# Performance work log

Measured on AMD Instinct MI355X. Metric: run time of the kernel, lower is better.

The kernel has to match this reference:

```python
import jax, jax.numpy as jnp
import numpy as np

B, D, SLOTS, TOPK, CODE, ANCH = 8192, 64, 32, 3, 128, 32
BETA = 0.25  # vq_commitment_beta


def _clinear(zr, zi, Wr, Wi, br, bi):
    # ComplexLinear: real = Wr(zr)-Wi(zi), imag = Wi(zr)+Wr(zi); each nn.Linear carries its own bias
    return (zr @ Wr + br) - (zi @ Wi + bi), (zr @ Wi + bi) + (zi @ Wr + br)


def _layernorm(x, g, b, eps=1e-6):
    m = x.mean(-1, keepdims=True)
    v = ((x - m) ** 2).mean(-1, keepdims=True)  # biased var, as torch LayerNorm
    return (x - m) / jnp.sqrt(v + eps) * g + b


def setup_inputs() -> dict:
    key = jax.random.key(0)
    ks = jax.random.split(key, 16)
    f = jax.random.normal
    s = 0.05
    rng_init = 1.0 / np.sqrt(D)
    return dict(
        curr_r=f(ks[0], (B, D)), curr_i=f(ks[1], (B, D)),
        mem_r=f(ks[2], (B, SLOTS, D)), mem_i=f(ks[3], (B, SLOTS, D)),
        codebook=jax.random.uniform(ks[4], (CODE, 2 * D), minval=-rng_init, maxval=rng_init),
        qkv_Wr=f(ks[5], (3, D, D)) * s, qkv_Wi=f(ks[6], (3, D, D)) * s,
        qkv_br=jnp.zeros((3, D)), qkv_bi=jnp.zeros((3, D)),
        quad_Wr=f(ks[7], (D, D)) * s, quad_Wi=f(ks[8], (D, D)) * s,
        quad_br=jnp.zeros((D,)), quad_bi=jnp.zeros((D,)),
        sens_Wr=f(ks[9], (D, D)) * s, sens_Wi=f(ks[10], (D, D)) * s,
        sens_br=jnp.zeros((D,)), sens_bi=jnp.zeros((D,)),
        vis_palette=f(ks[11], (ANCH, 2 * D)), aud_palette=f(ks[12], (ANCH, 2 * D)),
        gate_W=f(ks[13], (2 * D, 1)) * s, gate_b=jnp.zeros((1,)),
        addr_W=f(ks[14], (2 * D, SLOTS)) * s, addr_b=jnp.zeros((SLOTS,)),
        ln_gamma_r=jnp.ones((D,)), ln_beta_r=jnp.zeros((D,)),
        ln_gamma_i=jnp.ones((D,)), ln_beta_i=jnp.zeros((D,)),
    )


def reference(curr_r, curr_i, mem_r, mem_i, codebook,
              qkv_Wr, qkv_Wi, qkv_br, qkv_bi,
              quad_Wr, quad_Wi, quad_br, quad_bi,
              sens_Wr, sens_Wi, sens_br, sens_bi,
              vis_palette, aud_palette,
              gate_W, gate_b, addr_W, addr_b,
              ln_gamma_r, ln_beta_r, ln_gamma_i, ln_beta_i):
    sg = jax.lax.stop_gradient
    z_flat = jnp.concatenate([curr_r, curr_i], -1)  # [B,2D]

    # ---- EMA_VQ (eval path): argmin codebook lookup + straight-through ----
    d = (z_flat ** 2).sum(1, keepdims=True) + (codebook ** 2).sum(1) - 2.0 * z_flat @ codebook.T
    d = jnp.maximum(d, 0.0)
    indices = jnp.argmin(d, -1)                      # [B]
    z_q = codebook[indices]                          # [B,2D]
    vq_loss = BETA * ((sg(z_q) - z_flat) ** 2).mean(-1)
    z_q = z_flat + sg(z_q - z_flat)
    probs = jnp.zeros((CODE,), z_flat.dtype).at[indices].add(1.0) / B
    norm_entropy = -(probs * jnp.log(probs + 1e-10)).sum() / np.log(CODE)
    vq_r, vq_i = z_q[..., :D], z_q[..., D:]

    # ---- HermitianGating ----
    qr, qi = _clinear(curr_r, curr_i, qkv_Wr[0], qkv_Wi[0], qkv_br[0], qkv_bi[0])
    kr, ki = _clinear(curr_r, curr_i, qkv_Wr[1], qkv_Wi[1], qkv_br[1], qkv_bi[1])
    vr, vi = _clinear(curr_r, curr_i, qkv_Wr[2], qkv_Wi[2], qkv_br[2], qkv_bi[2])
    gate = jax.nn.sigmoid((qr * kr + qi * ki).sum(-1, keepdims=True))
    g_r, g_i = vr * gate, vi * gate

    # ---- AssociativeMemory: softmax read + topk scatter write ----
    sim = jnp.einsum('bsd,bd->bs', mem_r, curr_r) + jnp.einsum('bsd,bd->bs', mem_i, curr_i)
    sim = sim - sg(sim.max(-1, keepdims=True))
    attn = jax.nn.softmax(sim, -1)
    read_r = jnp.einsum('bs,bsd->bd', attn, mem_r)
    read_i = jnp.einsum('bs,bsd->bd', attn, mem_i)
    write_gate = jax.nn.sigmoid(z_flat @ gate_W + gate_b)[:, :, None]  # [B,1,1]
    logits = z_flat @ addr_W + addr_b
    logits = logits - sg(logits.max(-1, keepdims=True))
    ww = jax.nn.softmax(logits, -1)                  # [B,SLOTS]
    slot_entropy = (-(ww * jnp.log(ww + 1e-10)).sum(-1)).mean()
    top_vals, top_idx = jax.lax.top_k(ww, TOPK)
    sparse = jnp.zeros_like(ww).at[jnp.arange(B)[:, None], top_idx].set(top_vals)
    sparse = sparse / (sparse.sum(-1, keepdims=True) + 1e-6)
    eff = write_gate * sparse[..., None]             # [B,SLOTS,1]
    nm_r = jnp.tanh(mem_r + eff * (curr_r[:, None, :] - mem_r))
    nm_i = jnp.tanh(mem_i + eff * (curr_i[:, None, :] - mem_i))
    nm_r = _layernorm(nm_r, ln_gamma_r, ln_beta_r)
    nm_i = _layernorm(nm_i, ln_gamma_i, ln_beta_i)

    # ---- SubmodalityAnchorModule ----
    s_r, s_i = _clinear(curr_r, curr_i, sens_Wr, sens_Wi, sens_br, sens_bi)
    sflat = jnp.concatenate([s_r, s_i], -1)

    def attend(pal):
        sc = sflat @ pal.T
        sc = sc - sg(sc.max(-1, keepdims=True))
        return jax.nn.softmax(sc, -1) @ pal

    vis = attend(vis_palette)
    aud = attend(aud_palette)
    exp_r = vis[..., :D] - aud[..., D:]   # vis_c + i*aud_c
    exp_i = vis[..., D:] + aud[..., :D]

    # ---- QuadratureModule: multiply by i ----
    zr, zi = _clinear(curr_r, curr_i, quad_Wr, quad_Wi, quad_br, quad_bi)
    q_r, q_i = -zi, zr

    combined = jnp.concatenate(
        [vq_r, vq_i, g_r, g_i, read_r, read_i, exp_r, exp_i, q_r, q_i,
         nm_r.reshape(B, -1), nm_i.reshape(B, -1)], -1)  # [B, 10*D + 2*SLOTS*D]
    return combined, vq_loss, indices, slot_entropy, norm_entropy
```

## Files before the change

### kernel.cpp

```cpp
#include <hip/hip_runtime.h>
#include <hip/hip_bf16.h>


#define NROWS 8
#define NBLOCKS 1024
#define RSTRIDE 4736

static constexpr size_t OFF_VQLOSS = 38797312UL;
static constexpr size_t OFF_IDX    = 38805504UL;
static constexpr size_t OFF_SENT   = 38813696UL;
static constexpr size_t OFF_NENT   = 38813697UL;

struct Params {
  const float* curr_r; const float* curr_i;
  const float* mem_r;  const float* mem_i;
  const float* codebook;
  const float* qkv_Wr; const float* qkv_Wi; const float* qkv_br; const float* qkv_bi;
  const float* quad_Wr; const float* quad_Wi; const float* quad_br; const float* quad_bi;
  const float* sens_Wr; const float* sens_Wi; const float* sens_br; const float* sens_bi;
  const float* vis_pal; const float* aud_pal;
  const float* gate_W; const float* gate_b;
  const float* addr_W; const float* addr_b;
  const float* ln_gr; const float* ln_br; const float* ln_gi; const float* ln_bi;
  float* out;
  int* hist;
  float* rowent;
};

__global__ __launch_bounds__(256) void row_main(Params P) {
  const int b = blockIdx.x;
  const int t = threadIdx.x;
  const int lane = t & 63;
  const int wv = t >> 6;

  __shared__ float zr[64], zi[64];
  __shared__ float s_qr[64], s_qi[64], s_kr[64], s_ki[64], s_vr[64], s_vi[64];
  __shared__ float sfl[128];
  __shared__ float s_sp[4][4][64];
  __shared__ float lp[4][32];
  __shared__ float s_eff[32];
  __shared__ float s_sim[32], s_attn[32];
  __shared__ float s_rr[4][8][8], s_ri[4][8][8];
  __shared__ float s_pv[4][32], s_pa[4][32];
  __shared__ float s_pvp[32], s_pap[32];
  __shared__ float s_vo[128], s_ao[128];
  __shared__ float s_wg, s_gate;

  const size_t bb = (size_t)b;
  const int s = t >> 3, k = t & 7, d0 = k * 8;
  const float* mrp = P.mem_r + ((bb * 32 + s) * 64 + d0);
  const float* mip = P.mem_i + ((bb * 32 + s) * 64 + d0);
  float4 a0 = *(const float4*)mrp, a1 = *(const float4*)(mrp + 4);
  float4 b0 = *(const float4*)mip, b1 = *(const float4*)(mip + 4);
  float mr[8] = {a0.x, a0.y, a0.z, a0.w, a1.x, a1.y, a1.z, a1.w};
  float mi[8] = {b0.x, b0.y, b0.z, b0.w, b1.x, b1.y, b1.z, b1.w};

  if (t < 64)       zr[t]      = P.curr_r[bb * 64 + t];
  else if (t < 128) zi[t - 64] = P.curr_i[bb * 64 + (t - 64)];
  __syncthreads();

  float* orow = P.out + bb * RSTRIDE;

  {
    const int j = lane, cl = wv;
    const float *Wr, *Wi, *br_, *bi_;
    if      (cl == 0) { Wr = P.qkv_Wr;        Wi = P.qkv_Wi;        br_ = P.qkv_br;       bi_ = P.qkv_bi;       }
    else if (cl == 1) { Wr = P.qkv_Wr + 4096; Wi = P.qkv_Wi + 4096; br_ = P.qkv_br + 64;  bi_ = P.qkv_bi + 64;  }
    else if (cl == 2) { Wr = P.qkv_Wr + 8192; Wi = P.qkv_Wi + 8192; br_ = P.qkv_br + 128; bi_ = P.qkv_bi + 128; }
    else              { Wr = P.quad_Wr;       Wi = P.quad_Wi;       br_ = P.quad_br;      bi_ = P.quad_bi;      }
    float aRR = 0.f, aRI = 0.f, aIR = 0.f, aII = 0.f;
    for (int d = 0; d < 64; ++d) {
      const float xr = zr[d], xi = zi[d];
      const float wr = Wr[d * 64 + j], wi = Wi[d * 64 + j];
      aRR += xr * wr; aRI += xr * wi; aIR += xi * wr; aII += xi * wi;
    }
    const float oR = (aRR + br_[j]) - (aII + bi_[j]);
    const float oI = (aRI + bi_[j]) + (aIR + br_[j]);
    if      (cl == 0) { s_qr[j] = oR; s_qi[j] = oI; }
    else if (cl == 1) { s_kr[j] = oR; s_ki[j] = oI; }
    else if (cl == 2) { s_vr[j] = oR; s_vi[j] = oI; }
    else              { orow[512 + j] = -oI; orow[576 + j] = oR; }
    float bRR = 0.f, bRI = 0.f, bIR = 0.f, bII = 0.f;
    for (int dd = 0; dd < 16; ++dd) {
      const int d = wv * 16 + dd;
      const float xr = zr[d], xi = zi[d];
      const float wr = P.sens_Wr[d * 64 + j], wi = P.sens_Wi[d * 64 + j];
      bRR += xr * wr; bRI += xr * wi; bIR += xi * wr; bII += xi * wi;
    }
    s_sp[wv][0][j] = bRR; s_sp[wv][1][j] = bRI; s_sp[wv][2][j] = bIR; s_sp[wv][3][j] = bII;
  }
  __syncthreads();

  {
    float sp = 0.f;
    #pragma unroll
    for (int x = 0; x < 8; ++x) sp += mr[x] * zr[d0 + x] + mi[x] * zi[d0 + x];
    sp += __shfl_xor(sp, 1); sp += __shfl_xor(sp, 2); sp += __shfl_xor(sp, 4);
    if (k == 0) s_sim[s] = sp;
  }
  if (t < 128) {
    const int q = t >> 5, l = t & 31;
    const float* zz = (q < 2) ? zr : zi;
    const int zb = (q & 1) * 32;
    float a = 0.f;
    for (int i = 0; i < 32; ++i) a += zz[zb + i] * P.addr_W[(q * 32 + i) * 32 + l];
    lp[q][l] = a;
  } else if (t < 192) {
    const int j = t - 128;
    float tw = zr[j] * P.gate_W[j] + zi[j] * P.gate_W[64 + j];
    #pragma unroll
    for (int m = 1; m <= 32; m <<= 1) tw += __shfl_xor(tw, m);
    if (j == 0) s_wg = tw;
  } else {
    const int j = t - 192;
    float g = s_qr[j] * s_kr[j] + s_qi[j] * s_ki[j];
    #pragma unroll
    for (int m = 1; m <= 32; m <<= 1) g += __shfl_xor(g, m);
    if (j == 0) s_gate = 1.f / (1.f + expf(-g));
  }
  __syncthreads();

  if (t < 32) {
    float v = s_sim[t];
    float mx = v;
    #pragma unroll
    for (int m = 16; m >= 1; m >>= 1) mx = fmaxf(mx, __shfl_xor(mx, m));
    float e = expf(v - mx);
    float sm = e;
    #pragma unroll
    for (int m = 16; m >= 1; m >>= 1) sm += __shfl_xor(sm, m);
    s_attn[t] = e / sm;
  } else if (t >= 64 && t < 96) {
    const int l = t - 64;
    float lg = lp[0][l] + lp[1][l] + lp[2][l] + lp[3][l] + P.addr_b[l];
    float mx = lg;
    #pragma unroll
    for (int m = 16; m >= 1; m >>= 1) mx = fmaxf(mx, __shfl_xor(mx, m));
    float e = expf(lg - mx);
    float sm = e;
    #pragma unroll
    for (int m = 16; m >= 1; m >>= 1) sm += __shfl_xor(sm, m);
    const float w = e / sm;
    float es = -(w * logf(w + 1e-10f));
    #pragma unroll
    for (int m = 16; m >= 1; m >>= 1) es += __shfl_xor(es, m);
    if (l == 0) P.rowent[b] = es;
    const float myw = w;
    bool picked = false;
    float val = w; int idx = l;
    float sumtop = 0.f;
    #pragma unroll
    for (int it = 0; it < 3; ++it) {
      float v2 = val; int i2 = idx;
      #pragma unroll
      for (int m = 16; m >= 1; m >>= 1) {
        float ov = __shfl_xor(v2, m); int oi = __shfl_xor(i2, m);
        if (ov > v2 || (ov == v2 && oi < i2)) { v2 = ov; i2 = oi; }
      }
      sumtop += v2;
      if (l == i2) { picked = true; val = -1e30f; }
    }
    const float wgate = 1.f / (1.f + expf(-(s_wg + P.gate_b[0])));
    s_eff[l] = picked ? wgate * (myw / (sumtop + 1e-6f)) : 0.f;
  } else if (t >= 128 && t < 192) {
    const int j = t - 128;
    const float aRR = s_sp[0][0][j] + s_sp[1][0][j] + s_sp[2][0][j] + s_sp[3][0][j];
    const float aRI = s_sp[0][1][j] + s_sp[1][1][j] + s_sp[2][1][j] + s_sp[3][1][j];
    const float aIR = s_sp[0][2][j] + s_sp[1][2][j] + s_sp[2][2][j] + s_sp[3][2][j];
    const float aII = s_sp[0][3][j] + s_sp[1][3][j] + s_sp[2][3][j] + s_sp[3][3][j];
    const float oR = (aRR + P.sens_br[j]) - (aII + P.sens_bi[j]);
    const float oI = (aRI + P.sens_bi[j]) + (aIR + P.sens_br[j]);
    sfl[j] = oR; sfl[64 + j] = oI;
  }
  __syncthreads();

  const float aw = s_attn[s];
  {
    float pr[8], pi[8];
    #pragma unroll
    for (int x = 0; x < 8; ++x) { pr[x] = aw * mr[x]; pi[x] = aw * mi[x]; }
    #pragma unroll
    for (int m = 8; m <= 32; m <<= 1) {
      #pragma unroll
      for (int x = 0; x < 8; ++x) { pr[x] += __shfl_xor(pr[x], m); pi[x] += __shfl_xor(pi[x], m); }
    }
    if (lane < 8) {
      #pragma unroll
      for (int x = 0; x < 8; ++x) { s_rr[wv][lane][x] = pr[x]; s_ri[wv][lane][x] = pi[x]; }
    }
  }
  {
    const float eff = s_eff[s];
    float nr[8], ni[8];
    #pragma unroll
    for (int x = 0; x < 8; ++x) {
      nr[x] = tanhf(mr[x] + eff * (zr[d0 + x] - mr[x]));
      ni[x] = tanhf(mi[x] + eff * (zi[d0 + x] - mi[x]));
    }
    float sR = 0.f, sI = 0.f;
    #pragma unroll
    for (int x = 0; x < 8; ++x) { sR += nr[x]; sI += ni[x]; }
    sR += __shfl_xor(sR, 1); sR += __shfl_xor(sR, 2); sR += __shfl_xor(sR, 4);
    sI += __shfl_xor(sI, 1); sI += __shfl_xor(sI, 2); sI += __shfl_xor(sI, 4);
    const float mR = sR * (1.f / 64.f), mI = sI * (1.f / 64.f);
    float vR = 0.f, vI = 0.f;
    #pragma unroll
    for (int x = 0; x < 8; ++x) {
      float dr = nr[x] - mR; vR += dr * dr;
      float di = ni[x] - mI; vI += di * di;
    }
    vR += __shfl_xor(vR, 1); vR += __shfl_xor(vR, 2); vR += __shfl_xor(vR, 4);
    vI += __shfl_xor(vI, 1); vI += __shfl_xor(vI, 2); vI += __shfl_xor(vI, 4);
    const float invR = 1.f / sqrtf(vR * (1.f / 64.f) + 1e-6f);
    const float invI = 1.f / sqrtf(vI * (1.f / 64.f) + 1e-6f);
    float oR[8], oI[8];
    #pragma unroll
    for (int x = 0; x < 8; ++x) {
      const int d = d0 + x;
      oR[x] = (nr[x] - mR) * invR * P.ln_gr[d] + P.ln_br[d];
      oI[x] = (ni[x] - mI) * invI * P.ln_gi[d] + P.ln_bi[d];
    }
    *(float4*)&orow[640 + s * 64 + d0]      = make_float4(oR[0], oR[1], oR[2], oR[3]);
    *(float4*)&orow[640 + s * 64 + d0 + 4]  = make_float4(oR[4], oR[5], oR[6], oR[7]);
    *(float4*)&orow[2688 + s * 64 + d0]     = make_float4(oI[0], oI[1], oI[2], oI[3]);
    *(float4*)&orow[2688 + s * 64 + d0 + 4] = make_float4(oI[4], oI[5], oI[6], oI[7]);
  }
  if (t < 128) {
    const int a = t & 31, q = t >> 5;
    float sc = 0.f;
    for (int x = q * 32; x < q * 32 + 32; ++x) sc += sfl[x] * P.vis_pal[a * 128 + x];
    s_pv[q][a] = sc;
  } else {
    const int tt = t - 128, a = tt & 31, q = tt >> 5;
    float sc = 0.f;
    for (int x = q * 32; x < q * 32 + 32; ++x) sc += sfl[x] * P.aud_pal[a * 128 + x];
    s_pa[q][a] = sc;
  }
  __syncthreads();

  if (t < 64) {
    const int kk = t >> 3, xx = t & 7;
    float rv = s_rr[0][kk][xx] + s_rr[1][kk][xx] + s_rr[2][kk][xx] + s_rr[3][kk][xx];
    float iv = s_ri[0][kk][xx] + s_ri[1][kk][xx] + s_ri[2][kk][xx] + s_ri[3][kk][xx];
    orow[256 + t] = rv;
    orow[320 + t] = iv;
  } else if (t >= 128 && t < 160) {
    const int a = t - 128;
    float sc = s_pv[0][a] + s_pv[1][a] + s_pv[2][a] + s_pv[3][a];
    float mx = sc;
    #pragma unroll
    for (int m = 16; m >= 1; m >>= 1) mx = fmaxf(mx, __shfl_xor(mx, m));
    float e = expf(sc - mx);
    float sm = e;
    #pragma unroll
    for (int m = 16; m >= 1; m >>= 1) sm += __shfl_xor(sm, m);
    s_pvp[a] = e / sm;
  } else if (t >= 192 && t < 224) {
    const int a = t - 192;
    float sc = s_pa[0][a] + s_pa[1][a] + s_pa[2][a] + s_pa[3][a];
    float mx = sc;
    #pragma unroll
    for (int m = 16; m >= 1; m >>= 1) mx = fmaxf(mx, __shfl_xor(mx, m));
    float e = expf(sc - mx);
    float sm = e;
    #pragma unroll
    for (int m = 16; m >= 1; m >>= 1) sm += __shfl_xor(sm, m);
    s_pap[a] = e / sm;
  }
  __syncthreads();

  if (t < 128) {
    float v = 0.f;
    for (int a = 0; a < 32; ++a) v += s_pvp[a] * P.vis_pal[a * 128 + t];
    s_vo[t] = v;
  } else {
    const int j = t - 128;
    float v = 0.f;
    for (int a = 0; a < 32; ++a) v += s_pap[a] * P.aud_pal[a * 128 + j];
    s_ao[j] = v;
  }
  if (t < 64)       orow[128 + t] = s_vr[t] * s_gate;
  else if (t < 128) orow[192 + (t - 64)] = s_vi[t - 64] * s_gate;
  __syncthreads();

  if (t < 64)       orow[384 + t] = s_vo[t] - s_ao[64 + t];
  else if (t < 128) orow[448 + (t - 64)] = s_vo[t] + s_ao[t - 64];
}

__global__ __launch_bounds__(256) void vq_kernel(Params P) {
  const int t = threadIdx.x;
  const int bid = blockIdx.x;
  const int lane = t & 63;
  const int wv = t >> 6;

  __shared__ __align__(16) float s_zr[NROWS][64], s_zi[NROWS][64];
  __shared__ double s_cbn[128];
  __shared__ double s_dall[NROWS][256];
  __shared__ float s_vqls[NROWS];
  __shared__ int s_idx[NROWS];

  {
    const float* cr = P.curr_r + (size_t)bid * (NROWS * 64);
    const float* ci = P.curr_i + (size_t)bid * (NROWS * 64);
    float* zr = &s_zr[0][0];
    float* zi = &s_zi[0][0];
    for (int i = t; i < NROWS * 64; i += 256) { zr[i] = cr[i]; zi[i] = ci[i]; }
  }
  {
    const float* cb = P.codebook + (t & 127) * 128 + (t >> 7) * 64;
    double a = 0.0;
    for (int d = 0; d < 64; ++d) { double w = (double)cb[d]; a = fma(w, w, a); }
    s_dall[0][t] = a;
    __syncthreads();
    if (t < 128) s_cbn[t] = s_dall[0][t] + s_dall[0][t + 128];
    __syncthreads();
  }
  {
    const int c = t & 127, h = t >> 7;
    const float* cb = P.codebook + c * 128 + h * 64;
    const float (*zb)[64] = h ? s_zi : s_zr;
    double acc[NROWS];
    #pragma unroll
    for (int r = 0; r < NROWS; ++r) acc[r] = 0.0;
    for (int d = 0; d < 64; ++d) {
      const double w = (double)cb[d];
      #pragma unroll
      for (int r = 0; r < NROWS; ++r) acc[r] = fma(w, (double)zb[r][d], acc[r]);
    }
    #pragma unroll
    for (int r = 0; r < NROWS; ++r) s_dall[r][h * 128 + c] = acc[r];
    __syncthreads();
    #pragma unroll
    for (int rr = 0; rr < 2; ++rr) {
      const int r = wv * 2 + rr;
      const double d0 = s_cbn[lane]      - 2.0 * (s_dall[r][lane]      + s_dall[r][128 + lane]);
      const double d1 = s_cbn[lane + 64] - 2.0 * (s_dall[r][64 + lane] + s_dall[r][192 + lane]);
      double sv = d0; int si = lane;
      if (d1 < sv) { sv = d1; si = lane + 64; }
      #pragma unroll
      for (int m = 1; m <= 32; m <<= 1) {
        double ov = __shfl_xor(sv, m);
        int oi = __shfl_xor(si, m);
        if (ov < sv || (ov == sv && oi < si)) { sv = ov; si = oi; }
      }
      if (lane == 0) { s_idx[r] = si; atomicAdd(&P.hist[si], 1); }
    }
    __syncthreads();
  }
  {
    #pragma unroll
    for (int rr = 0; rr < 2; ++rr) {
      const int r = wv * 2 + rr;
      const float* cb = P.codebook + (size_t)s_idx[r] * 128;
      float d0_ = cb[lane] - s_zr[r][lane];
      float d1_ = cb[64 + lane] - s_zi[r][lane];
      float v = d0_ * d0_ + d1_ * d1_;
      #pragma unroll
      for (int m = 1; m <= 32; m <<= 1) v += __shfl_xor(v, m);
      if (lane == 0) s_vqls[r] = 0.25f * v * (1.0f / 128.0f);
    }
  }
  __syncthreads();
  {
    const int j = t & 63, g = t >> 6;
    #pragma unroll
    for (int rr = 0; rr < 4; ++rr) {
      const int r = (g >> 1) * 4 + rr;
      float* orow = P.out + ((size_t)bid * NROWS + r) * RSTRIDE;
      const float* cb = P.codebook + (size_t)s_idx[r] * 128;
      if ((g & 1) == 0) {
        float z = s_zr[r][j];
        orow[j] = z + (cb[j] - z);
      } else {
        float z = s_zi[r][j];
        orow[64 + j] = z + (cb[64 + j] - z);
      }
    }
  }
  if (t < NROWS) {
    P.out[OFF_VQLOSS + (size_t)bid * NROWS + t] = s_vqls[t];
    P.out[OFF_IDX + (size_t)bid * NROWS + t] = (float)s_idx[t];
  }
}

__global__ __launch_bounds__(256) void finalize_k(const int* hist, const float* rowent,
                                                  float* out) {
  const int t = threadIdx.x;
  __shared__ float red[256];
  float se = 0.f;
  for (int i = t; i < 8192; i += 256) se += rowent[i];
  red[t] = se;
  __syncthreads();
  for (int off = 128; off >= 1; off >>= 1) {
    if (t < off) red[t] += red[t + off];
    __syncthreads();
  }
  if (t == 0) out[OFF_SENT] = red[0] / 8192.0f;
  __syncthreads();
  float ne = 0.f;
  if (t < 128) {
    const float pp = (float)hist[t] / 8192.0f;
    ne = -(pp * logf(pp + 1e-10f));
  }
  red[t] = ne;
  __syncthreads();
  for (int off = 128; off >= 1; off >>= 1) {
    if (t < off) red[t] += red[t + off];
    __syncthreads();
  }
  if (t == 0) out[OFF_NENT] = red[0] / logf(128.0f);
}

extern "C" void kernel_launch(void* const* d_in, const int* in_sizes, int n_in,
                              void* d_out, int out_size, void* d_ws, size_t ws_size,
                              hipStream_t stream) {
  (void)in_sizes; (void)n_in; (void)out_size; (void)ws_size;
  Params P;
  P.curr_r   = (const float*)d_in[0];
  P.curr_i   = (const float*)d_in[1];
  P.mem_r    = (const float*)d_in[2];
  P.mem_i    = (const float*)d_in[3];
  P.codebook = (const float*)d_in[4];
  P.qkv_Wr   = (const float*)d_in[5];
  P.qkv_Wi   = (const float*)d_in[6];
  P.qkv_br   = (const float*)d_in[7];
  P.qkv_bi   = (const float*)d_in[8];
  P.quad_Wr  = (const float*)d_in[9];
  P.quad_Wi  = (const float*)d_in[10];
  P.quad_br  = (const float*)d_in[11];
  P.quad_bi  = (const float*)d_in[12];
  P.sens_Wr  = (const float*)d_in[13];
  P.sens_Wi  = (const float*)d_in[14];
  P.sens_br  = (const float*)d_in[15];
  P.sens_bi  = (const float*)d_in[16];
  P.vis_pal  = (const float*)d_in[17];
  P.aud_pal  = (const float*)d_in[18];
  P.gate_W   = (const float*)d_in[19];
  P.gate_b   = (const float*)d_in[20];
  P.addr_W   = (const float*)d_in[21];
  P.addr_b   = (const float*)d_in[22];
  P.ln_gr    = (const float*)d_in[23];
  P.ln_br    = (const float*)d_in[24];
  P.ln_gi    = (const float*)d_in[25];
  P.ln_bi    = (const float*)d_in[26];
  P.out = (float*)d_out;
  P.hist = (int*)d_ws;
  P.rowent = (float*)((char*)d_ws + 512);

  hipMemsetAsync(d_ws, 0, 512, stream);
  row_main<<<dim3(8192), dim3(256), 0, stream>>>(P);
  vq_kernel<<<dim3(NBLOCKS), dim3(256), 0, stream>>>(P);
  finalize_k<<<dim3(1), dim3(256), 0, stream>>>(P.hist, P.rowent, (float*)d_out);
}
```

Measured before the change: 252.3 us.

## Fuse VQ kernel into per-row kernel processing two rows per block

Result: slower. 277.2 us (+9.9%).

```diff
diff --git a/kernel.cpp b/kernel.cpp
--- a/kernel.cpp
+++ b/kernel.cpp
@@ -2,8 +2,6 @@
 #include <hip/hip_bf16.h>
 
 
-#define NROWS 8
-#define NBLOCKS 1024
 #define RSTRIDE 4736
 
 static constexpr size_t OFF_VQLOSS = 38797312UL;
@@ -27,40 +25,109 @@
   float* rowent;
 };
 
-__global__ __launch_bounds__(256) void row_main(Params P) {
+__global__ __launch_bounds__(256) void row2_kernel(Params P) {
   const int b = blockIdx.x;
   const int t = threadIdx.x;
   const int lane = t & 63;
   const int wv = t >> 6;
 
-  __shared__ float zr[64], zi[64];
-  __shared__ float s_qr[64], s_qi[64], s_kr[64], s_ki[64], s_vr[64], s_vi[64];
-  __shared__ float sfl[128];
-  __shared__ float s_sp[4][4][64];
-  __shared__ float lp[4][32];
-  __shared__ float s_eff[32];
-  __shared__ float s_sim[32], s_attn[32];
-  __shared__ float s_rr[4][8][8], s_ri[4][8][8];
-  __shared__ float s_pv[4][32], s_pa[4][32];
-  __shared__ float s_pvp[32], s_pap[32];
-  __shared__ float s_vo[128], s_ao[128];
-  __shared__ float s_wg, s_gate;
-
-  const size_t bb = (size_t)b;
+  __shared__ float zr[2][64], zi[2][64];
+  __shared__ double s_pd[2][2][128];
+  __shared__ float s_qr[2][64], s_qi[2][64], s_kr[2][64], s_ki[2][64], s_vr[2][64], s_vi[2][64];
+  __shared__ float sfl[2][128];
+  __shared__ float s_sp[4][2][4][64];
+  __shared__ float alg[2][32];
+  __shared__ float s_eff[2][32];
+  __shared__ float s_sim[2][32], s_attn[2][32];
+  __shared__ float s_rr[2][4][8][8], s_ri[2][4][8][8];
+  __shared__ float s_pv[2][4][32], s_pa[2][4][32];
+  __shared__ float s_pvp[2][32], s_pap[2][32];
+  __shared__ float s_vo[2][128], s_ao[2][128];
+  __shared__ float s_wg[2], s_gate[2], s_vqls[2];
+  __shared__ int s_idx[2];
+
+  const size_t r0 = (size_t)b * 2;
+  float* orow0 = P.out + r0 * RSTRIDE;
+  float* orow1 = P.out + (r0 + 1) * RSTRIDE;
+
   const int s = t >> 3, k = t & 7, d0 = k * 8;
-  const float* mrp = P.mem_r + ((bb * 32 + s) * 64 + d0);
-  const float* mip = P.mem_i + ((bb * 32 + s) * 64 + d0);
-  float4 a0 = *(const float4*)mrp, a1 = *(const float4*)(mrp + 4);
-  float4 b0 = *(const float4*)mip, b1 = *(const float4*)(mip + 4);
-  float mr[8] = {a0.x, a0.y, a0.z, a0.w, a1.x, a1.y, a1.z, a1.w};
-  float mi[8] = {b0.x, b0.y, b0.z, b0.w, b1.x, b1.y, b1.z, b1.w};
-
-  if (t < 64)       zr[t]      = P.curr_r[bb * 64 + t];
-  else if (t < 128) zi[t - 64] = P.curr_i[bb * 64 + (t - 64)];
-  __syncthreads();
-
-  float* orow = P.out + bb * RSTRIDE;
-
+  const float* mrp0 = P.mem_r + ((r0)     * 32 + s) * 64 + d0;
+  const float* mip0 = P.mem_i + ((r0)     * 32 + s) * 64 + d0;
+  const float* mrp1 = P.mem_r + ((r0 + 1) * 32 + s) * 64 + d0;
+  const float* mip1 = P.mem_i + ((r0 + 1) * 32 + s) * 64 + d0;
+  float4 a00 = *(const float4*)mrp0, a01 = *(const float4*)(mrp0 + 4);
+  float4 b00 = *(const float4*)mip0, b01 = *(const float4*)(mip0 + 4);
+  float4 a10 = *(const float4*)mrp1, a11 = *(const float4*)(mrp1 + 4);
+  float4 b10 = *(const float4*)mip1, b11 = *(const float4*)(mip1 + 4);
+  float mr0[8] = {a00.x, a00.y, a00.z, a00.w, a01.x, a01.y, a01.z, a01.w};
+  float mi0[8] = {b00.x, b00.y, b00.z, b00.w, b01.x, b01.y, b01.z, b01.w};
+  float mr1[8] = {a10.x, a10.y, a10.z, a10.w, a11.x, a11.y, a11.z, a11.w};
+  float mi1[8] = {b10.x, b10.y, b10.z, b10.w, b11.x, b11.y, b11.z, b11.w};
+
+  if (t < 128) zr[t >> 6][t & 63] = P.curr_r[r0 * 64 + t];
+  else         zi[(t - 128) >> 6][t & 63] = P.curr_i[r0 * 64 + (t - 128)];
+  __syncthreads();
+
+  {
+    const int c = t & 127, h = t >> 7;
+    const float* cb = P.codebook + (size_t)c * 128 + h * 64;
+    const float* z0 = h ? zi[0] : zr[0];
+    const float* z1 = h ? zi[1] : zr[1];
+    double a0 = 0.0, a1 = 0.0;
+    for (int x = 0; x < 64; ++x) {
+      const double w = (double)cb[x];
+      const double e0 = w - (double)z0[x]; a0 = fma(e0, e0, a0);
+      const double e1 = w - (double)z1[x]; a1 = fma(e1, e1, a1);
+    }
+    s_pd[h][0][c] = a0;
+    s_pd[h][1][c] = a1;
+  }
+  __syncthreads();
+
+  if (wv < 2) {
+    const int r = wv;
+    double sv = s_pd[0][r][lane] + s_pd[1][r][lane]; int si = lane;
+    const double dv = s_pd[0][r][lane + 64] + s_pd[1][r][lane + 64];
+    if (dv < sv) { sv = dv; si = lane + 64; }
+    #pragma unroll
+    for (int m = 1; m <= 32; m <<= 1) {
+      double ov = __shfl_xor(sv, m);
+      int oi = __shfl_xor(si, m);
+      if (ov < sv || (ov == sv && oi < si)) { sv = ov; si = oi; }
+    }
+    if (lane == 0) { s_idx[r] = si; atomicAdd(&P.hist[si], 1); }
+  } else if (wv == 2) {
+    const int r = lane >> 5, l = lane & 31;
+    float wg = 0.f;
+    #pragma unroll
+    for (int q4 = 0; q4 < 4; ++q4) {
+      const int jj = l + q4 * 32;
+      const float z = (jj < 64) ? zr[r][jj] : zi[r][jj - 64];
+      wg += z * P.gate_W[jj];
+    }
+    #pragma unroll
+    for (int m = 16; m >= 1; m >>= 1) wg += __shfl_xor(wg, m);
+    if (l == 0) s_wg[r] = wg;
+  } else {
+    const int r = lane >> 5, l = lane & 31;
+    float a = P.addr_b[l];
+    for (int d = 0; d < 64; ++d) a += zr[r][d] * P.addr_W[d * 32 + l];
+    for (int d = 0; d < 64; ++d) a += zi[r][d] * P.addr_W[(64 + d) * 32 + l];
+    alg[r][l] = a;
+  }
+  __syncthreads();
+
+  {
+    float sp0 = 0.f, sp1 = 0.f;
+    #pragma unroll
+    for (int x = 0; x < 8; ++x) {
+      sp0 += mr0[x] * zr[0][d0 + x] + mi0[x] * zi[0][d0 + x];
+      sp1 += mr1[x] * zr[1][d0 + x] + mi1[x] * zi[1][d0 + x];
+    }
+    sp0 += __shfl_xor(sp0, 1); sp0 += __shfl_xor(sp0, 2); sp0 += __shfl_xor(sp0, 4);
+    sp1 += __shfl_xor(sp1, 1); sp1 += __shfl_xor(sp1, 2); sp1 += __shfl_xor(sp1, 4);
+    if (k == 0) { s_sim[0][s] = sp0; s_sim[1][s] = sp1; }
+  }
   {
     const int j = lane, cl = wv;
     const float *Wr, *Wi, *br_, *bi_;
@@ -68,71 +135,66 @@
     else if (cl == 1) { Wr = P.qkv_Wr + 4096; Wi = P.qkv_Wi + 4096; br_ = P.qkv_br + 64;  bi_ = P.qkv_bi + 64;  }
     else if (cl == 2) { Wr = P.qkv_Wr + 8192; Wi = P.qkv_Wi + 8192; br_ = P.qkv_br + 128; bi_ = P.qkv_bi + 128; }
     else              { Wr = P.quad_Wr;       Wi = P.quad_Wi;       br_ = P.quad_br;      bi_ = P.quad_bi;      }
-    float aRR = 0.f, aRI = 0.f, aIR = 0.f, aII = 0.f;
+    float aRR0 = 0.f, aRI0 = 0.f, aIR0 = 0.f, aII0 = 0.f;
+    float aRR1 = 0.f, aRI1 = 0.f, aIR1 = 0.f, aII1 = 0.f;
     for (int d = 0; d < 64; ++d) {
-      const float xr = zr[d], xi = zi[d];
       const float wr = Wr[d * 64 + j], wi = Wi[d * 64 + j];
-      aRR += xr * wr; aRI += xr * wi; aIR += xi * wr; aII += xi * wi;
-    }
-    const float oR = (aRR + br_[j]) - (aII + bi_[j]);
-    const float oI = (aRI + bi_[j]) + (aIR + br_[j]);
-    if      (cl == 0) { s_qr[j] = oR; s_qi[j] = oI; }
-    else if (cl == 1) { s_kr[j] = oR; s_ki[j] = oI; }
-    else if (cl == 2) { s_vr[j] = oR; s_vi[j] = oI; }
-    else              { orow[512 + j] = -oI; orow[576 + j] = oR; }
-    float bRR = 0.f, bRI = 0.f, bIR = 0.f, bII = 0.f;
+      const float xr0 = zr[0][d], xi0 = zi[0][d];
+      const float xr1 = zr[1][d], xi1 = zi[1][d];
+      aRR0 += xr0 * wr; aRI0 += xr0 * wi; aIR0 += xi0 * wr; aII0 += xi0 * wi;
+      aRR1 += xr1 * wr; aRI1 += xr1 * wi; aIR1 += xi1 * wr; aII1 += xi1 * wi;
+    }
+    const float brj = br_[j], bij = bi_[j];
+    const float oR0 = (aRR0 + brj) - (aII0 + bij);
+    const float oI0 = (aRI0 + bij) + (aIR0 + brj);
+    const float oR1 = (aRR1 + brj) - (aII1 + bij);
+    const float oI1 = (aRI1 + bij) + (aIR1 + brj);
+    if      (cl == 0) { s_qr[0][j] = oR0; s_qi[0][j] = oI0; s_qr[1][j] = oR1; s_qi[1][j] = oI1; }
+    else if (cl == 1) { s_kr[0][j] = oR0; s_ki[0][j] = oI0; s_kr[1][j] = oR1; s_ki[1][j] = oI1; }
+    else if (cl == 2) { s_vr[0][j] = oR0; s_vi[0][j] = oI0; s_vr[1][j] = oR1; s_vi[1][j] = oI1; }
+    else { orow0[512 + j] = -oI0; orow0[576 + j] = oR0;
+           orow1[512 + j] = -oI1; orow1[576 + j] = oR1; }
+    float bRR0 = 0.f, bRI0 = 0.f, bIR0 = 0.f, bII0 = 0.f;
+    float bRR1 = 0.f, bRI1 = 0.f, bIR1 = 0.f, bII1 = 0.f;
     for (int dd = 0; dd < 16; ++dd) {
       const int d = wv * 16 + dd;
-      const float xr = zr[d], xi = zi[d];
       const float wr = P.sens_Wr[d * 64 + j], wi = P.sens_Wi[d * 64 + j];
-      bRR += xr * wr; bRI += xr * wi; bIR += xi * wr; bII += xi * wi;
-    }
-    s_sp[wv][0][j] = bRR; s_sp[wv][1][j] = bRI; s_sp[wv][2][j] = bIR; s_sp[wv][3][j] = bII;
-  }
-  __syncthreads();
-
-  {
-    float sp = 0.f;
-    #pragma unroll
-    for (int x = 0; x < 8; ++x) sp += mr[x] * zr[d0 + x] + mi[x] * zi[d0 + x];
-    sp += __shfl_xor(sp, 1); sp += __shfl_xor(sp, 2); sp += __shfl_xor(sp, 4);
-    if (k == 0) s_sim[s] = sp;
-  }
-  if (t < 128) {
-    const int q = t >> 5, l = t & 31;
-    const float* zz = (q < 2) ? zr : zi;
-    const int zb = (q & 1) * 32;
-    float a = 0.f;
-    for (int i = 0; i < 32; ++i) a += zz[zb + i] * P.addr_W[(q * 32 + i) * 32 + l];
-    lp[q][l] = a;
-  } else if (t < 192) {
-    const int j = t - 128;
-    float tw = zr[j] * P.gate_W[j] + zi[j] * P.gate_W[64 + j];
-    #pragma unroll
-    for (int m = 1; m <= 32; m <<= 1) tw += __shfl_xor(tw, m);
-    if (j == 0) s_wg = tw;
-  } else {
-    const int j = t - 192;
-    float g = s_qr[j] * s_kr[j] + s_qi[j] * s_ki[j];
-    #pragma unroll
-    for (int m = 1; m <= 32; m <<= 1) g += __shfl_xor(g, m);
-    if (j == 0) s_gate = 1.f / (1.f + expf(-g));
-  }
-  __syncthreads();
-
-  if (t < 32) {
-    float v = s_sim[t];
-    float mx = v;
-    #pragma unroll
-    for (int m = 16; m >= 1; m >>= 1) mx = fmaxf(mx, __shfl_xor(mx, m));
-    float e = expf(v - mx);
-    float sm = e;
-    #pragma unroll
-    for (int m = 16; m >= 1; m >>= 1) sm += __shfl_xor(sm, m);
-    s_attn[t] = e / sm;
-  } else if (t >= 64 && t < 96) {
-    const int l = t - 64;
-    float lg = lp[0][l] + lp[1][l] + lp[2][l] + lp[3][l] + P.addr_b[l];
+      const float xr0 = zr[0][d], xi0 = zi[0][d];
+      const float xr1 = zr[1][d], xi1 = zi[1][d];
+      bRR0 += xr0 * wr; bRI0 += xr0 * wi; bIR0 += xi0 * wr; bII0 += xi0 * wi;
+      bRR1 += xr1 * wr; bRI1 += xr1 * wi; bIR1 += xi1 * wr; bII1 += xi1 * wi;
+    }
+    s_sp[wv][0][0][j] = bRR0; s_sp[wv][0][1][j] = bRI0; s_sp[wv][0][2][j] = bIR0; s_sp[wv][0][3][j] = bII0;
+    s_sp[wv][1][0][j] = bRR1; s_sp[wv][1][1][j] = bRI1; s_sp[wv][1][2][j] = bIR1; s_sp[wv][1][3][j] = bII1;
+  }
+  __syncthreads();
+
+  if (wv == 0) {
+    {
+      const int r = lane >> 5, l = lane & 31;
+      float v = s_sim[r][l];
+      float mx = v;
+      #pragma unroll
+      for (int m = 16; m >= 1; m >>= 1) mx = fmaxf(mx, __shfl_xor(mx, m));
+      float e = expf(v - mx);
+      float sm = e;
+      #pragma unroll
+      for (int m = 16; m >= 1; m >>= 1) sm += __shfl_xor(sm, m);
+      s_attn[r][l] = e / sm;
+    }
+    #pragma unroll
+    for (int r2 = 0; r2 < 2; ++r2) {
+      const float* cb = P.codebook + (size_t)s_idx[r2] * 128;
+      const float d0_ = cb[lane] - zr[r2][lane];
+      const float d1_ = cb[64 + lane] - zi[r2][lane];
+      float v2 = d0_ * d0_ + d1_ * d1_;
+      #pragma unroll
+      for (int m = 1; m <= 32; m <<= 1) v2 += __shfl_xor(v2, m);
+      if (lane == 0) s_vqls[r2] = 0.25f * v2 * (1.0f / 128.0f);
+    }
+  } else if (wv == 1) {
+    const int r = lane >> 5, l = lane & 31;
+    float lg = alg[r][l];
     float mx = lg;
     #pragma unroll
     for (int m = 16; m >= 1; m >>= 1) mx = fmaxf(mx, __shfl_xor(mx, m));
@@ -144,7 +206,7 @@
     float es = -(w * logf(w + 1e-10f));
     #pragma unroll
     for (int m = 16; m >= 1; m >>= 1) es += __shfl_xor(es, m);
-    if (l == 0) P.rowent[b] = es;
+    if (l == 0) P.rowent[r0 + r] = es;
     const float myw = w;
     bool picked = false;
     float val = w; int idx = l;
@@ -160,25 +222,34 @@
       sumtop += v2;
       if (l == i2) { picked = true; val = -1e30f; }
     }
-    const float wgate = 1.f / (1.f + expf(-(s_wg + P.gate_b[0])));
-    s_eff[l] = picked ? wgate * (myw / (sumtop + 1e-6f)) : 0.f;
-  } else if (t >= 128 && t < 192) {
-    const int j = t - 128;
-    const float aRR = s_sp[0][0][j] + s_sp[1][0][j] + s_sp[2][0][j] + s_sp[3][0][j];
-    const float aRI = s_sp[0][1][j] + s_sp[1][1][j] + s_sp[2][1][j] + s_sp[3][1][j];
-    const float aIR = s_sp[0][2][j] + s_sp[1][2][j] + s_sp[2][2][j] + s_sp[3][2][j];
-    const float aII = s_sp[0][3][j] + s_sp[1][3][j] + s_sp[2][3][j] + s_sp[3][3][j];
+    const float wgate = 1.f / (1.f + expf(-(s_wg[r] + P.gate_b[0])));
+    s_eff[r][l] = picked ? wgate * (myw / (sumtop + 1e-6f)) : 0.f;
+  } else {
+    const int r = wv - 2;
+    const int j = lane;
+    const float aRR = s_sp[0][r][0][j] + s_sp[1][r][0][j] + s_sp[2][r][0][j] + s_sp[3][r][0][j];
+    const float aRI = s_sp[0][r][1][j] + s_sp[1][r][1][j] + s_sp[2][r][1][j] + s_sp[3][r][1][j];
+    const float aIR = s_sp[0][r][2][j] + s_sp[1][r][2][j] + s_sp[2][r][2][j] + s_sp[3][r][2][j];
+    const float aII = s_sp[0][r][3][j] + s_sp[1][r][3][j] + s_sp[2][r][3][j] + s_sp[3][r][3][j];
     const float oR = (aRR + P.sens_br[j]) - (aII + P.sens_bi[j]);
     const float oI = (aRI + P.sens_bi[j]) + (aIR + P.sens_br[j]);
-    sfl[j] = oR; sfl[64 + j] = oI;
-  }
-  __syncthreads();
-
-  const float aw = s_attn[s];
-  {
+    sfl[r][j] = oR; sfl[r][64 + j] = oI;
+    if (lane < 32) {
+      const int l = lane;
+      float g = s_qr[r][l] * s_kr[r][l] + s_qi[r][l] * s_ki[r][l]
+              + s_qr[r][l + 32] * s_kr[r][l + 32] + s_qi[r][l + 32] * s_ki[r][l + 32];
+      #pragma unroll
+      for (int m = 16; m >= 1; m >>= 1) g += __shfl_xor(g, m);
+      if (l == 0) s_gate[r] = 1.f / (1.f + expf(-g));
+    }
+  }
+  __syncthreads();
+
+  {
+    const float aw0 = s_attn[0][s], aw1 = s_attn[1][s];
     float pr[8], pi[8];
     #pragma unroll
-    for (int x = 0; x < 8; ++x) { pr[x] = aw * mr[x]; pi[x] = aw * mi[x]; }
+    for (int x = 0; x < 8; ++x) { pr[x] = aw0 * mr0[x]; pi[x] = aw0 * mi0[x]; }
     #pragma unroll
     for (int m = 8; m <= 32; m <<= 1) {
       #pragma unroll
@@ -186,16 +257,31 @@
     }
     if (lane < 8) {
       #pragma unroll
-      for (int x = 0; x < 8; ++x) { s_rr[wv][lane][x] = pr[x]; s_ri[wv][lane][x] = pi[x]; }
-    }
-  }
-  {
-    const float eff = s_eff[s];
+      for (int x = 0; x < 8; ++x) { s_rr[0][wv][lane][x] = pr[x]; s_ri[0][wv][lane][x] = pi[x]; }
+    }
+    #pragma unroll
+    for (int x = 0; x < 8; ++x) { pr[x] = aw1 * mr1[x]; pi[x] = aw1 * mi1[x]; }
+    #pragma unroll
+    for (int m = 8; m <= 32; m <<= 1) {
+      #pragma unroll
+      for (int x = 0; x < 8; ++x) { pr[x] += __shfl_xor(pr[x], m); pi[x] += __shfl_xor(pi[x], m); }
+    }
+    if (lane < 8) {
+      #pragma unroll
+      for (int x = 0; x < 8; ++x) { s_rr[1][wv][lane][x] = pr[x]; s_ri[1][wv][lane][x] = pi[x]; }
+    }
+  }
+  #pragma unroll
+  for (int r = 0; r < 2; ++r) {
+    const float eff = s_eff[r][s];
+    const float* mrx = r ? mr1 : mr0;
+    const float* mix = r ? mi1 : mi0;
+    float* orow = r ? orow1 : orow0;
     float nr[8], ni[8];
     #pragma unroll
     for (int x = 0; x < 8; ++x) {
-      nr[x] = tanhf(mr[x] + eff * (zr[d0 + x] - mr[x]));
-      ni[x] = tanhf(mi[x] + eff * (zi[d0 + x] - mi[x]));
+      nr[x] = tanhf(mrx[x] + eff * (zr[r][d0 + x] - mrx[x]));
+      ni[x] = tanhf(mix[x] + eff * (zi[r][d0 + x] - mix[x]));
     }
     float sR = 0.f, sI = 0.f;
     #pragma unroll
@@ -206,8 +292,8 @@
     float vR = 0.f, vI = 0.f;
     #pragma unroll
     for (int x = 0; x < 8; ++x) {
-      float dr = nr[x] - mR; vR += dr * dr;
-      float di = ni[x] - mI; vI += di * di;
+      const float dr = nr[x] - mR; vR += dr * dr;
+      const float di = ni[x] - mI; vI += di * di;
     }
     vR += __shfl_xor(vR, 1); vR += __shfl_xor(vR, 2); vR += __shfl_xor(vR, 4);
     vI += __shfl_xor(vI, 1); vI += __shfl_xor(vI, 2); vI += __shfl_xor(vI, 4);
@@ -225,28 +311,29 @@
     *(float4*)&orow[2688 + s * 64 + d0]     = make_float4(oI[0], oI[1], oI[2], oI[3]);
     *(float4*)&orow[2688 + s * 64 + d0 + 4] = make_float4(oI[4], oI[5], oI[6], oI[7]);
   }
+  {
+    const float* sf = sfl[t >> 7];
+    const int a = t & 31, q = (t >> 5) & 3;
+    float sc = 0.f, sa = 0.f;
+    for (int x = q * 32; x < q * 32 + 32; ++x) {
+      sc += sf[x] * P.vis_pal[a * 128 + x];
+      sa += sf[x] * P.aud_pal[a * 128 + x];
+    }
+    s_pv[t >> 7][q][a] = sc;
+    s_pa[t >> 7][q][a] = sa;
+  }
+  __syncthreads();
+
   if (t < 128) {
-    const int a = t & 31, q = t >> 5;
-    float sc = 0.f;
-    for (int x = q * 32; x < q * 32 + 32; ++x) sc += sfl[x] * P.vis_pal[a * 128 + x];
-    s_pv[q][a] = sc;
-  } else {
-    const int tt = t - 128, a = tt & 31, q = tt >> 5;
-    float sc = 0.f;
-    for (int x = q * 32; x < q * 32 + 32; ++x) sc += sfl[x] * P.aud_pal[a * 128 + x];
-    s_pa[q][a] = sc;
-  }
-  __syncthreads();
-
-  if (t < 64) {
-    const int kk = t >> 3, xx = t & 7;
-    float rv = s_rr[0][kk][xx] + s_rr[1][kk][xx] + s_rr[2][kk][xx] + s_rr[3][kk][xx];
-    float iv = s_ri[0][kk][xx] + s_ri[1][kk][xx] + s_ri[2][kk][xx] + s_ri[3][kk][xx];
-    orow[256 + t] = rv;
-    orow[320 + t] = iv;
-  } else if (t >= 128 && t < 160) {
-    const int a = t - 128;
-    float sc = s_pv[0][a] + s_pv[1][a] + s_pv[2][a] + s_pv[3][a];
+    const int r = t >> 6, tt = t & 63, kk = tt >> 3, xx = tt & 7;
+    const float rv = s_rr[r][0][kk][xx] + s_rr[r][1][kk][xx] + s_rr[r][2][kk][xx] + s_rr[r][3][kk][xx];
+    const float iv = s_ri[r][0][kk][xx] + s_ri[r][1][kk][xx] + s_ri[r][2][kk][xx] + s_ri[r][3][kk][xx];
+    float* orow = r ? orow1 : orow0;
+    orow[256 + tt] = rv;
+    orow[320 + tt] = iv;
+  } else if (wv == 2) {
+    const int r = lane >> 5, a = lane & 31;
+    float sc = s_pv[r][0][a] + s_pv[r][1][a] + s_pv[r][2][a] + s_pv[r][3][a];
     float mx = sc;
     #pragma unroll
     for (int m = 16; m >= 1; m >>= 1) mx = fmaxf(mx, __shfl_xor(mx, m));
@@ -254,10 +341,10 @@
     float sm = e;
     #pragma unroll
     for (int m = 16; m >= 1; m >>= 1) sm += __shfl_xor(sm, m);
-    s_pvp[a] = e / sm;
-  } else if (t >= 192 && t < 224) {
-    const int a = t - 192;
-    float sc = s_pa[0][a] + s_pa[1][a] + s_pa[2][a] + s_pa[3][a];
+    s_pvp[r][a] = e / sm;
+  } else {
+    const int r = lane >> 5, a = lane & 31;
+    float sc = s_pa[r][0][a] + s_pa[r][1][a] + s_pa[r][2][a] + s_pa[r][3][a];
     float mx = sc;
     #pragma unroll
     for (int m = 16; m >= 1; m >>= 1) mx = fmaxf(mx, __shfl_xor(mx, m));
@@ -265,121 +352,37 @@
     float sm = e;
     #pragma unroll
     for (int m = 16; m >= 1; m >>= 1) sm += __shfl_xor(sm, m);
-    s_pap[a] = e / sm;
-  }
-  __syncthreads();
-
-  if (t < 128) {
-    float v = 0.f;
-    for (int a = 0; a < 32; ++a) v += s_pvp[a] * P.vis_pal[a * 128 + t];
-    s_vo[t] = v;
-  } else {
-    const int j = t - 128;
-    float v = 0.f;
-    for (int a = 0; a < 32; ++a) v += s_pap[a] * P.aud_pal[a * 128 + j];
-    s_ao[j] = v;
-  }
-  if (t < 64)       orow[128 + t] = s_vr[t] * s_gate;
-  else if (t < 128) orow[192 + (t - 64)] = s_vi[t - 64] * s_gate;
-  __syncthreads();
-
-  if (t < 64)       orow[384 + t] = s_vo[t] - s_ao[64 + t];
-  else if (t < 128) orow[448 + (t - 64)] = s_vo[t] + s_ao[t - 64];
-}
-
-__global__ __launch_bounds__(256) void vq_kernel(Params P) {
-  const int t = threadIdx.x;
-  const int bid = blockIdx.x;
-  const int lane = t & 63;
-  const int wv = t >> 6;
-
-  __shared__ __align__(16) float s_zr[NROWS][64], s_zi[NROWS][64];
-  __shared__ double s_cbn[128];
-  __shared__ double s_dall[NROWS][256];
-  __shared__ float s_vqls[NROWS];
-  __shared__ int s_idx[NROWS];
-
-  {
-    const float* cr = P.curr_r + (size_t)bid * (NROWS * 64);
-    const float* ci = P.curr_i + (size_t)bid * (NROWS * 64);
-    float* zr = &s_zr[0][0];
-    float* zi = &s_zi[0][0];
-    for (int i = t; i < NROWS * 64; i += 256) { zr[i] = cr[i]; zi[i] = ci[i]; }
-  }
-  {
-    const float* cb = P.codebook + (t & 127) * 128 + (t >> 7) * 64;
-    double a = 0.0;
-    for (int d = 0; d < 64; ++d) { double w = (double)cb[d]; a = fma(w, w, a); }
-    s_dall[0][t] = a;
-    __syncthreads();
-    if (t < 128) s_cbn[t] = s_dall[0][t] + s_dall[0][t + 128];
-    __syncthreads();
-  }
-  {
-    const int c = t & 127, h = t >> 7;
-    const float* cb = P.codebook + c * 128 + h * 64;
-    const float (*zb)[64] = h ? s_zi : s_zr;
-    double acc[NROWS];
-    #pragma unroll
-    for (int r = 0; r < NROWS; ++r) acc[r] = 0.0;
-    for (int d = 0; d < 64; ++d) {
-      const double w = (double)cb[d];
-      #pragma unroll
-      for (int r = 0; r < NROWS; ++r) acc[r] = fma(w, (double)zb[r][d], acc[r]);
-    }
-    #pragma unroll
-    for (int r = 0; r < NROWS; ++r) s_dall[r][h * 128 + c] = acc[r];
-    __syncthreads();
-    #pragma unroll
-    for (int rr = 0; rr < 2; ++rr) {
-      const int r = wv * 2 + rr;
-      const double d0 = s_cbn[lane]      - 2.0 * (s_dall[r][lane]      + s_dall[r][128 + lane]);
-      const double d1 = s_cbn[lane + 64] - 2.0 * (s_dall[r][64 + lane] + s_dall[r][192 + lane]);
-      double sv = d0; int si = lane;
-      if (d1 < sv) { sv = d1; si = lane + 64; }
-      #pragma unroll
-      for (int m = 1; m <= 32; m <<= 1) {
-        double ov = __shfl_xor(sv, m);
-        int oi = __shfl_xor(si, m);
-        if (ov < sv || (ov == sv && oi < si)) { sv = ov; si = oi; }
-      }
-      if (lane == 0) { s_idx[r] = si; atomicAdd(&P.hist[si], 1); }
-    }
-    __syncthreads();
-  }
-  {
-    #pragma unroll
-    for (int rr = 0; rr < 2; ++rr) {
-      const int r = wv * 2 + rr;
-      const float* cb = P.codebook + (size_t)s_idx[r] * 128;
-      float d0_ = cb[lane] - s_zr[r][lane];
-      float d1_ = cb[64 + lane] - s_zi[r][lane];
-      float v = d0_ * d0_ + d1_ * d1_;
-      #pragma unroll
-      for (int m = 1; m <= 32; m <<= 1) v += __shfl_xor(v, m);
-      if (lane == 0) s_vqls[r] = 0.25f * v * (1.0f / 128.0f);
-    }
-  }
-  __syncthreads();
-  {
-    const int j = t & 63, g = t >> 6;
-    #pragma unroll
-    for (int rr = 0; rr < 4; ++rr) {
-      const int r = (g >> 1) * 4 + rr;
-      float* orow = P.out + ((size_t)bid * NROWS + r) * RSTRIDE;
-      const float* cb = P.codebook + (size_t)s_idx[r] * 128;
-      if ((g & 1) == 0) {
-        float z = s_zr[r][j];
-        orow[j] = z + (cb[j] - z);
-      } else {
-        float z = s_zi[r][j];
-        orow[64 + j] = z + (cb[64 + j] - z);
-      }
-    }
-  }
-  if (t < NROWS) {
-    P.out[OFF_VQLOSS + (size_t)bid * NROWS + t] = s_vqls[t];
-    P.out[OFF_IDX + (size_t)bid * NROWS + t] = (float)s_idx[t];
+    s_pap[r][a] = e / sm;
+  }
+  __syncthreads();
+
+  {
+    const int r = t >> 7, j = t & 127;
+    float v = 0.f, w2 = 0.f;
+    for (int a = 0; a < 32; ++a) {
+      v  += s_pvp[r][a] * P.vis_pal[a * 128 + j];
+      w2 += s_pap[r][a] * P.aud_pal[a * 128 + j];
+    }
+    s_vo[r][j] = v;
+    s_ao[r][j] = w2;
+    float* orow = r ? orow1 : orow0;
+    if (j < 64) orow[128 + j] = s_vr[r][j] * s_gate[r];
+    else        orow[192 + (j - 64)] = s_vi[r][j - 64] * s_gate[r];
+  }
+  __syncthreads();
+
+  {
+    const int r = t >> 7, j = t & 127;
+    float* orow = r ? orow1 : orow0;
+    if (j < 64) orow[384 + j] = s_vo[r][j] - s_ao[r][64 + j];
+    else        orow[448 + (j - 64)] = s_vo[r][j] + s_ao[r][j - 64];
+    const float* cb = P.codebook + (size_t)s_idx[r] * 128;
+    const float z = (j < 64) ? zr[r][j] : zi[r][j - 64];
+    orow[j] = z + (cb[j] - z);
+  }
+  if (t < 2) {
+    P.out[OFF_VQLOSS + r0 + t] = s_vqls[t];
+    P.out[OFF_IDX + r0 + t] = (float)s_idx[t];
   }
 }
 
@@ -448,7 +451,6 @@
   P.rowent = (float*)((char*)d_ws + 512);
 
   hipMemsetAsync(d_ws, 0, 512, stream);
-  row_main<<<dim3(8192), dim3(256), 0, stream>>>(P);
-  vq_kernel<<<dim3(NBLOCKS), dim3(256), 0, stream>>>(P);
+  row2_kernel<<<dim3(4096), dim3(256), 0, stream>>>(P);
   finalize_k<<<dim3(1), dim3(256), 0, stream>>>(P.hist, P.rowent, (float*)d_out);
 }
```
